# Kernel tuning notes

Measured on AMD Instinct MI355X. Metric: run time of the kernel, lower is better.

## Reference

```python
import jax, jax.numpy as jnp
import numpy as np

N_NODES = 50000
N_EDGES = 1600000
F_IN = 128
C = 64          # block in/out channels
EF = 64         # edge MLP hidden dim
BLOCKS = 3
MLP_DIM = 128
N_CLASSES = 10
N_GRAPHS = 512
EPS = 1e-5


def setup_inputs() -> dict:
    key = jax.random.key(0)
    ks = jax.random.split(key, 32)
    s = 0.05
    inp = {
        "x": jax.random.normal(ks[0], (N_NODES, F_IN), jnp.float32),
        "edge_index": jax.random.randint(ks[1], (2, N_EDGES), 0, N_NODES, jnp.int64),
        "batch": jnp.sort(jax.random.randint(ks[2], (N_NODES,), 0, N_GRAPHS, jnp.int64)),
        "fc0_w": jax.random.normal(ks[3], (F_IN, C), jnp.float32) * s,
        "fc0_b": jnp.zeros((C,), jnp.float32),
        "fc1_w": jax.random.normal(ks[4], (BLOCKS * C, MLP_DIM), jnp.float32) * s,
        "fc1_b": jnp.zeros((MLP_DIM,), jnp.float32),
        "fc2_w": jax.random.normal(ks[5], (MLP_DIM, N_CLASSES), jnp.float32) * s,
        "fc2_b": jnp.zeros((N_CLASSES,), jnp.float32),
    }
    for i in range(BLOCKS):
        k = 6 + 4 * i
        inp[f"bn_g{i}"] = jnp.ones((C,), jnp.float32)
        inp[f"bn_b{i}"] = jnp.zeros((C,), jnp.float32)
        inp[f"w1_{i}"] = jax.random.normal(ks[k], (2 * C, EF), jnp.float32) * s
        inp[f"b1_{i}"] = jnp.zeros((EF,), jnp.float32)
        inp[f"w2_{i}"] = jax.random.normal(ks[k + 1], (EF, C), jnp.float32) * s
        inp[f"b2_{i}"] = jnp.zeros((C,), jnp.float32)
    return inp


def _batchnorm(x, g, b):
    mu = jnp.mean(x, axis=0)
    var = jnp.var(x, axis=0)
    return (x - mu) * jax.lax.rsqrt(var + EPS) * g + b


def _edge_conv(x, src, dst, w1, b1, w2, b2):
    # PyG-style EdgeConv: msg = MLP(concat[x_i, x_j - x_i]), max-aggregate at i
    xi = x[dst]                                  # [E, C]
    xj = x[src]                                  # [E, C]
    h = jax.nn.relu(jnp.concatenate([xi, xj - xi], axis=-1) @ w1 + b1)  # [E, EF]
    m = h @ w2 + b2                              # [E, C]
    agg = jax.ops.segment_max(m, dst, num_segments=N_NODES)
    return jnp.where(jnp.isfinite(agg), agg, 0.0)


def reference(x, edge_index, batch, fc0_w, fc0_b, fc1_w, fc1_b, fc2_w, fc2_b,
              bn_g0, bn_b0, w1_0, b1_0, w2_0, b2_0,
              bn_g1, bn_b1, w1_1, b1_1, w2_1, b2_1,
              bn_g2, bn_b2, w1_2, b1_2, w2_2, b2_2):
    src, dst = edge_index[0], edge_index[1]
    h = x @ fc0_w + fc0_b                        # [N, C]
    blocks = [(bn_g0, bn_b0, w1_0, b1_0, w2_0, b2_0),
              (bn_g1, bn_b1, w1_1, b1_1, w2_1, b2_1),
              (bn_g2, bn_b2, w1_2, b1_2, w2_2, b2_2)]
    xs = []
    for (g, b, w1, b1, w2, b2) in blocks:
        h = _batchnorm(h, g, b)
        h = jax.nn.relu(_edge_conv(h, src, dst, w1, b1, w2, b2))
        xs.append(h)
    cat = jnp.concatenate(xs, axis=-1)           # [N, 3C]
    # global mean pool over graphs
    sums = jax.ops.segment_sum(cat, batch, num_segments=N_GRAPHS)
    cnt = jax.ops.segment_sum(jnp.ones((N_NODES,), cat.dtype), batch,
                              num_segments=N_GRAPHS)
    pooled = sums / jnp.maximum(cnt, 1.0)[:, None]   # [G, 3C]
    hid = jax.nn.relu(pooled @ fc1_w + fc1_b)
    return jax.nn.log_softmax(hid @ fc2_w + fc2_b, axis=-1)
```

## Files before the change

kernel.cpp:

```cpp
#include <hip/hip_runtime.h>
#include <math.h>

#define N_NODES 50000
#define N_TILES 3125
#define N_EDGES 1600000
#define F_IN 128
#define C 64
#define EF 64
#define N_GRAPHS 512
#define MLP_DIM 128
#define N_CLASSES 10
#define EPS 1e-5f
#define NB 196
#define CAPB 16384
#define CHUNK 4096
#define NSLICE 8

typedef __attribute__((ext_vector_type(8))) _Float16 half8;
typedef __attribute__((ext_vector_type(2))) _Float16 half2v;
typedef __attribute__((ext_vector_type(4))) float floatx4;
typedef __attribute__((ext_vector_type(4))) unsigned uintx4;

union Uh { uintx4 v; half2v h[4]; half8 h8; };

__device__ __forceinline__ unsigned short f2h(float a) {
    union { _Float16 f; unsigned short u; } c;
    c.f = (_Float16)a;
    return c.u;
}
__device__ __forceinline__ float h2f(unsigned short u) {
    union { unsigned short u; _Float16 f; } c;
    c.u = u;
    return (float)c.f;
}
__device__ __forceinline__ half2v pk2(float a, float b) {
    auto t = __builtin_amdgcn_cvt_pkrtz(a, b);
    union { decltype(t) i; half2v o; } c;
    c.i = t;
    return c.o;
}

__global__ __launch_bounds__(256) void pass1_kernel(const int* __restrict__ src,
                                                    const int* __restrict__ dst,
                                                    int* __restrict__ gcur,
                                                    unsigned* __restrict__ keys) {
    __shared__ int lcnt[NB], lbase[NB], lcnt2[NB];
    int tid = threadIdx.x;
    int e0 = blockIdx.x * CHUNK;
    unsigned k[CHUNK / 256];
    int bk[CHUNK / 256];
    for (int i = tid; i < NB; i += 256) lcnt[i] = 0;
    __syncthreads();
#pragma unroll
    for (int i = 0; i < CHUNK / 256; i++) {
        int e = e0 + i * 256 + tid;
        if (e < N_EDGES) {
            int d = dst[e];
            k[i] = ((unsigned)d << 16) | (unsigned)src[e];
            bk[i] = d >> 8;
            atomicAdd(&lcnt[bk[i]], 1);
        } else bk[i] = -1;
    }
    __syncthreads();
    for (int i = tid; i < NB; i += 256) {
        int c = lcnt[i];
        lbase[i] = c ? atomicAdd(&gcur[i], c) : 0;
        lcnt2[i] = 0;
    }
    __syncthreads();
#pragma unroll
    for (int i = 0; i < CHUNK / 256; i++) {
        if (bk[i] >= 0) {
            int r = atomicAdd(&lcnt2[bk[i]], 1);
            keys[(size_t)bk[i] * CAPB + lbase[bk[i]] + r] = k[i];
        }
    }
}

__global__ __launch_bounds__(256) void node_count_kernel(const unsigned* __restrict__ keys,
                                                         const int* __restrict__ bcnt,
                                                         int* __restrict__ cnt,
                                                         int* __restrict__ bsum) {
    __shared__ int lc[256], rs[256];
    int tid = threadIdx.x, b = blockIdx.x;
    lc[tid] = 0;
    __syncthreads();
    int beg = b * CAPB, end = beg + bcnt[b];
    for (int p = beg + tid; p < end; p += 256)
        atomicAdd(&lc[(keys[p] >> 16) & 255], 1);
    __syncthreads();
    int node = b * 256 + tid;
    int c = (node < N_NODES) ? lc[tid] : 0;
    if (node < N_NODES) cnt[node] = c;
    rs[tid] = (c + 15) & ~15;
    __syncthreads();
    for (int off = 128; off > 0; off >>= 1) {
        if (tid < off) rs[tid] += rs[tid + off];
        __syncthreads();
    }
    if (tid == 0) bsum[b] = rs[0];
}

__global__ void pscan_kernel(const int* __restrict__ bsum, int* __restrict__ bbase,
                             int* __restrict__ row_start) {
    __shared__ int a[256];
    int tid = threadIdx.x;
    int v = (tid < NB) ? bsum[tid] : 0;
    a[tid] = v;
    __syncthreads();
    for (int off = 1; off < 256; off <<= 1) {
        int t = (tid >= off) ? a[tid - off] : 0;
        __syncthreads();
        a[tid] += t;
        __syncthreads();
    }
    int excl = a[tid] - v;
    if (tid < NB) bbase[tid] = excl;
    if (tid == NB - 1) row_start[N_NODES] = excl + v;
}

__global__ __launch_bounds__(256) void pass2_kernel(const unsigned* __restrict__ keys,
                                                    const int* __restrict__ bcnt,
                                                    const int* __restrict__ cnt,
                                                    const int* __restrict__ bbase,
                                                    int* __restrict__ row_start,
                                                    unsigned short* __restrict__ sorted_src) {
    __shared__ int loc[256], rs[256], cur[256];
    int tid = threadIdx.x, b = blockIdx.x;
    int node = b * 256 + tid;
    int c = (node < N_NODES) ? cnt[node] : 0;
    int pc = (c + 15) & ~15;
    loc[tid] = pc;
    cur[tid] = 0;
    __syncthreads();
    for (int off = 1; off < 256; off <<= 1) {
        int t = (tid >= off) ? loc[tid - off] : 0;
        __syncthreads();
        loc[tid] += t;
        __syncthreads();
    }
    int myrs = bbase[b] + loc[tid] - pc;
    rs[tid] = myrs;
    if (node < N_NODES) row_start[node] = myrs;
    __syncthreads();
    int beg = b * CAPB, end = beg + bcnt[b];
    for (int p = beg + tid; p < end; p += 256) {
        unsigned k = keys[p];
        int lidx = (k >> 16) & 255;
        int r = atomicAdd(&cur[lidx], 1);
        sorted_src[rs[lidx] + r] = (unsigned short)(k & 0xFFFFu);
    }
    __syncthreads();
    if (node < N_NODES) {
        int deg = cur[tid];
        if (deg > 0) {
            unsigned short s0 = sorted_src[myrs];
            for (int p = myrs + deg; p < myrs + pc; p++) sorted_src[p] = s0;
        }
    }
}

__global__ __launch_bounds__(256, 3) void fc0_mfma_kernel(const float* __restrict__ x,
                                                          const float* __restrict__ w,
                                                          const float* __restrict__ b,
                                                          unsigned short* __restrict__ h0,
                                                          float* __restrict__ bns) {
    __shared__ float bl1[4][64], bl2[4][64];
    int tid = threadIdx.x, lane = tid & 63, wid = tid >> 6;
    int q = lane >> 4, cl = lane & 15, kq = q * 8;

    Uh wf[4][4];
#pragma unroll
    for (int kh = 0; kh < 4; kh++)
#pragma unroll
        for (int cb = 0; cb < 4; cb++)
#pragma unroll
            for (int j = 0; j < 4; j++) {
                int k0 = kh * 32 + kq + 2 * j;
                int col = cb * 16 + cl;
                wf[kh][cb].h[j] = pk2(w[k0 * 64 + col], w[(k0 + 1) * 64 + col]);
            }
    float bv[4];
#pragma unroll
    for (int cb = 0; cb < 4; cb++) bv[cb] = b[cb * 16 + cl];
    float s1[4] = {0, 0, 0, 0}, s2[4] = {0, 0, 0, 0};

    for (int t = blockIdx.x * 4 + wid; t < N_TILES; t += gridDim.x * 4) {
        int nb = t * 16;
        floatx4 acc[4] = {{0,0,0,0},{0,0,0,0},{0,0,0,0},{0,0,0,0}};
#pragma unroll
        for (int kh = 0; kh < 4; kh++) {
            const float* xr = x + (size_t)(nb + cl) * F_IN + kh * 32 + kq;
            floatx4 xa = *(const floatx4*)xr;
            floatx4 xb = *(const floatx4*)(xr + 4);
            Uh xf;
            xf.h[0] = pk2(xa.x, xa.y); xf.h[1] = pk2(xa.z, xa.w);
            xf.h[2] = pk2(xb.x, xb.y); xf.h[3] = pk2(xb.z, xb.w);
#pragma unroll
            for (int cb = 0; cb < 4; cb++)
                acc[cb] = __builtin_amdgcn_mfma_f32_16x16x32_f16(xf.h8, wf[kh][cb].h8, acc[cb], 0, 0, 0);
        }
#pragma unroll
        for (int cb = 0; cb < 4; cb++)
#pragma unroll
            for (int r = 0; r < 4; r++) {
                float v = acc[cb][r] + bv[cb];
                h0[(size_t)(nb + q * 4 + r) * 64 + cb * 16 + cl] = f2h(v);
                s1[cb] += v; s2[cb] += v * v;
            }
    }
#pragma unroll
    for (int cb = 0; cb < 4; cb++) {
        s1[cb] += __shfl_xor(s1[cb], 16); s1[cb] += __shfl_xor(s1[cb], 32);
        s2[cb] += __shfl_xor(s2[cb], 16); s2[cb] += __shfl_xor(s2[cb], 32);
    }
    if (lane < 16) {
#pragma unroll
        for (int cb = 0; cb < 4; cb++) { bl1[wid][cb * 16 + lane] = s1[cb]; bl2[wid][cb * 16 + lane] = s2[cb]; }
    }
    __syncthreads();
    if (tid < 64) {
        float a  = bl1[0][tid] + bl1[1][tid] + bl1[2][tid] + bl1[3][tid];
        float c2 = bl2[0][tid] + bl2[1][tid] + bl2[2][tid] + bl2[3][tid];
        int sl = blockIdx.x & (NSLICE - 1);
        atomicAdd(&bns[sl * 128 + tid], a);
        atomicAdd(&bns[sl * 128 + 64 + tid], c2);
    }
}

__global__ __launch_bounds__(256, 4) void ab_mfma_kernel(const unsigned short* __restrict__ h,
                                                         const float* __restrict__ bns,
                                                         const float* __restrict__ g,
                                                         const float* __restrict__ bb,
                                                         const float* __restrict__ w1,
                                                         const float* __restrict__ b1,
                                                         unsigned short* __restrict__ A,
                                                         unsigned short* __restrict__ Bb) {
    __shared__ float scale[64], shift[64], cab[128];
    int tid = threadIdx.x, lane = tid & 63, wid = tid >> 6;
    int q = lane >> 4, cl = lane & 15, kq = q * 8;

    if (tid < 64) {
        float s1v = 0.f, s2v = 0.f;
#pragma unroll
        for (int s = 0; s < NSLICE; s++) { s1v += bns[s * 128 + tid]; s2v += bns[s * 128 + 64 + tid]; }
        float mu  = s1v * (1.0f / N_NODES);
        float var = s2v * (1.0f / N_NODES) - mu * mu;
        float sc  = g[tid] * rsqrtf(var + EPS);
        scale[tid] = sc;
        shift[tid] = bb[tid] - mu * sc;
    }
    __syncthreads();
    if (tid < 128) {
        int j = tid & 63;
        float acc = (tid < 64) ? b1[j] : 0.f;
        for (int k = 0; k < 64; k++) {
            float wa_ = w1[k * EF + j], wb_ = w1[(64 + k) * EF + j];
            acc = fmaf(shift[k], (tid < 64) ? (wa_ - wb_) : wb_, acc);
        }
        cab[tid] = acc;
    }
    Uh wa[2][4], wb[2][4];
#pragma unroll
    for (int kh = 0; kh < 2; kh++)
#pragma unroll
        for (int cb = 0; cb < 4; cb++)
#pragma unroll
            for (int j = 0; j < 4; j++) {
                int k0 = kh * 32 + kq + 2 * j;
                int col = cb * 16 + cl;
                float sa = scale[k0], sb = scale[k0 + 1];
                float a0 = w1[k0 * EF + col], b0 = w1[(64 + k0) * EF + col];
                float a1 = w1[(k0 + 1) * EF + col], b1v = w1[(64 + k0 + 1) * EF + col];
                wa[kh][cb].h[j] = pk2(sa * (a0 - b0), sb * (a1 - b1v));
                wb[kh][cb].h[j] = pk2(sa * b0, sb * b1v);
            }
    __syncthreads();
    float cav[4], cbv[4];
#pragma unroll
    for (int cb = 0; cb < 4; cb++) { cav[cb] = cab[cb * 16 + cl]; cbv[cb] = cab[64 + cb * 16 + cl]; }

    for (int t = blockIdx.x * 4 + wid; t < N_TILES; t += gridDim.x * 4) {
        int nb = t * 16;
        const unsigned short* hrow = h + (size_t)(nb + cl) * 64 + kq;
        Uh h0f, h1f;
        h0f.v = *(const uintx4*)hrow;
        h1f.v = *(const uintx4*)(hrow + 32);
        floatx4 accA[4] = {{0,0,0,0},{0,0,0,0},{0,0,0,0},{0,0,0,0}};
        floatx4 accB[4] = {{0,0,0,0},{0,0,0,0},{0,0,0,0},{0,0,0,0}};
#pragma unroll
        for (int cb = 0; cb < 4; cb++) {
            accA[cb] = __builtin_amdgcn_mfma_f32_16x16x32_f16(h0f.h8, wa[0][cb].h8, accA[cb], 0, 0, 0);
            accB[cb] = __builtin_amdgcn_mfma_f32_16x16x32_f16(h0f.h8, wb[0][cb].h8, accB[cb], 0, 0, 0);
            accA[cb] = __builtin_amdgcn_mfma_f32_16x16x32_f16(h1f.h8, wa[1][cb].h8, accA[cb], 0, 0, 0);
            accB[cb] = __builtin_amdgcn_mfma_f32_16x16x32_f16(h1f.h8, wb[1][cb].h8, accB[cb], 0, 0, 0);
        }
#pragma unroll
        for (int cb = 0; cb < 4; cb++)
#pragma unroll
            for (int r = 0; r < 4; r++) {
                size_t o = (size_t)(nb + q * 4 + r) * 64 + cb * 16 + cl;
                A[o]  = f2h(accA[cb][r] + cav[cb]);
                Bb[o] = f2h(accB[cb][r] + cbv[cb]);
            }
    }
}

__global__ __launch_bounds__(256, 4) void edge_mfma_kernel(
        const unsigned short* __restrict__ A, const unsigned short* __restrict__ Bb,
        const int* __restrict__ row_start, const unsigned short* __restrict__ sorted_src,
        const float* __restrict__ w2, const float* __restrict__ b2,
        unsigned short* __restrict__ catp, float* __restrict__ bnsNext) {
    __shared__ float r1[4][64], r2[4][64];
    int tid = threadIdx.x, lane = tid & 63, wid = tid >> 6;
    int kq = (lane >> 4) * 8;
    int cl = lane & 15;

    Uh bfr[2][4];
#pragma unroll
    for (int kh = 0; kh < 2; kh++)
#pragma unroll
        for (int cb = 0; cb < 4; cb++)
#pragma unroll
            for (int j = 0; j < 4; j++) {
                _Float16 w0 = (_Float16)w2[(kh * 32 + kq + 2 * j) * 64 + cb * 16 + cl];
                _Float16 w1 = (_Float16)w2[(kh * 32 + kq + 2 * j + 1) * 64 + cb * 16 + cl];
                bfr[kh][cb].h[j] = half2v{w0, w1};
            }
    float b2j = b2[lane];
    float s1 = 0.f, s2 = 0.f;
    const half2v zeroh = {(_Float16)0.f, (_Float16)0.f};

    for (int n = blockIdx.x * 4 + wid; n < N_NODES; n += gridDim.x * 4) {
        int beg = row_start[n], end = row_start[n + 1];
        const unsigned short* arow = A + (size_t)n * 64 + kq;
        Uh a0u, a1u;
        a0u.v = *(const uintx4*)(arow);
        a1u.v = *(const uintx4*)(arow + 32);
        floatx4 rmax0 = {-INFINITY, -INFINITY, -INFINITY, -INFINITY};
        floatx4 rmax1 = rmax0, rmax2 = rmax0, rmax3 = rmax0;

        auto tile = [&](uintx4 u0, uintx4 u1) {
            Uh b0u, b1u, f0, f1;
            b0u.v = u0; b1u.v = u1;
#pragma unroll
            for (int j = 0; j < 4; j++) {
                f0.h[j] = __builtin_elementwise_max(a0u.h[j] + b0u.h[j], zeroh);
                f1.h[j] = __builtin_elementwise_max(a1u.h[j] + b1u.h[j], zeroh);
            }
            floatx4 acc0 = {0.f, 0.f, 0.f, 0.f}, acc1 = acc0, acc2 = acc0, acc3 = acc0;
            acc0 = __builtin_amdgcn_mfma_f32_16x16x32_f16(f0.h8, bfr[0][0].h8, acc0, 0, 0, 0);
            acc1 = __builtin_amdgcn_mfma_f32_16x16x32_f16(f0.h8, bfr[0][1].h8, acc1, 0, 0, 0);
            acc2 = __builtin_amdgcn_mfma_f32_16x16x32_f16(f0.h8, bfr[0][2].h8, acc2, 0, 0, 0);
            acc3 = __builtin_amdgcn_mfma_f32_16x16x32_f16(f0.h8, bfr[0][3].h8, acc3, 0, 0, 0);
            acc0 = __builtin_amdgcn_mfma_f32_16x16x32_f16(f1.h8, bfr[1][0].h8, acc0, 0, 0, 0);
            acc1 = __builtin_amdgcn_mfma_f32_16x16x32_f16(f1.h8, bfr[1][1].h8, acc1, 0, 0, 0);
            acc2 = __builtin_amdgcn_mfma_f32_16x16x32_f16(f1.h8, bfr[1][2].h8, acc2, 0, 0, 0);
            acc3 = __builtin_amdgcn_mfma_f32_16x16x32_f16(f1.h8, bfr[1][3].h8, acc3, 0, 0, 0);
            rmax0 = __builtin_elementwise_max(rmax0, acc0);
            rmax1 = __builtin_elementwise_max(rmax1, acc1);
            rmax2 = __builtin_elementwise_max(rmax2, acc2);
            rmax3 = __builtin_elementwise_max(rmax3, acc3);
        };
        auto gather = [&](int p, uintx4& u0, uintx4& u1) {
            int srcm = sorted_src[p + cl];
            const unsigned short* brow = Bb + (size_t)srcm * 64 + kq;
            u0 = *(const uintx4*)(brow);
            u1 = *(const uintx4*)(brow + 32);
        };

        int p0 = beg;
        for (; p0 + 32 <= end; p0 += 32) {
            uintx4 x0, x1, y0, y1;
            gather(p0, x0, x1);
            gather(p0 + 16, y0, y1);
            tile(x0, x1);
            tile(y0, y1);
        }
        if (p0 < end) {
            uintx4 x0, x1;
            gather(p0, x0, x1);
            tile(x0, x1);
        }

        float v0 = fmaxf(fmaxf(rmax0.x, rmax0.y), fmaxf(rmax0.z, rmax0.w));
        float v1 = fmaxf(fmaxf(rmax1.x, rmax1.y), fmaxf(rmax1.z, rmax1.w));
        float v2 = fmaxf(fmaxf(rmax2.x, rmax2.y), fmaxf(rmax2.z, rmax2.w));
        float v3 = fmaxf(fmaxf(rmax3.x, rmax3.y), fmaxf(rmax3.z, rmax3.w));
        v0 = fmaxf(v0, __shfl_xor(v0, 16)); v0 = fmaxf(v0, __shfl_xor(v0, 32));
        v1 = fmaxf(v1, __shfl_xor(v1, 16)); v1 = fmaxf(v1, __shfl_xor(v1, 32));
        v2 = fmaxf(v2, __shfl_xor(v2, 16)); v2 = fmaxf(v2, __shfl_xor(v2, 32));
        v3 = fmaxf(v3, __shfl_xor(v3, 16)); v3 = fmaxf(v3, __shfl_xor(v3, 32));
        float vs = (lane & 32) ? ((lane & 16) ? v3 : v2) : ((lane & 16) ? v1 : v0);
        float v = fmaxf(vs + b2j, 0.f);
        catp[(size_t)n * 64 + lane] = f2h(v);
        s1 += v; s2 += v * v;
    }

    if (bnsNext) {
        r1[wid][lane] = s1; r2[wid][lane] = s2;
        __syncthreads();
        if (tid < 64) {
            float a  = r1[0][tid] + r1[1][tid] + r1[2][tid] + r1[3][tid];
            float c2 = r2[0][tid] + r2[1][tid] + r2[2][tid] + r2[3][tid];
            int sl = blockIdx.x & (NSLICE - 1);
            atomicAdd(&bnsNext[sl * 128 + tid], a);
            atomicAdd(&bnsNext[sl * 128 + 64 + tid], c2);
        }
    }
}

__global__ __launch_bounds__(192) void poolhead_kernel(const unsigned short* __restrict__ cat0,
                                                       const unsigned short* __restrict__ cat1,
                                                       const unsigned short* __restrict__ cat2,
                                                       const int* __restrict__ batch,
                                                       const float* __restrict__ fc1w,
                                                       const float* __restrict__ fc1b,
                                                       const float* __restrict__ fc2w,
                                                       const float* __restrict__ fc2b,
                                                       float* __restrict__ out) {
    __shared__ int se[2];
    __shared__ float p[192];
    __shared__ float hid[128];
    __shared__ float z[10];
    __shared__ float lse;
    int g = blockIdx.x, tid = threadIdx.x;
    if (tid < 2) {
        int target = g + tid;
        int lo = 0, hi = N_NODES;
        while (lo < hi) { int mid = (lo + hi) >> 1; if (batch[mid] < target) lo = mid + 1; else hi = mid; }
        se[tid] = lo;
    }
    __syncthreads();
    int s = se[0], e = se[1];
    const unsigned short* plane = (tid < 64) ? cat0 : ((tid < 128) ? cat1 : cat2);
    int col = tid & 63;
    float acc = 0.f;
    for (int r = s; r < e; r++) acc += h2f(plane[(size_t)r * 64 + col]);
    float denom = (e > s) ? (float)(e - s) : 1.0f;
    p[tid] = acc / denom;
    __syncthreads();
    if (tid < MLP_DIM) {
        float a = fc1b[tid];
        for (int k = 0; k < 192; k++) a = fmaf(p[k], fc1w[k * 128 + tid], a);
        hid[tid] = fmaxf(a, 0.f);
    }
    __syncthreads();
    if (tid < N_CLASSES) {
        float a = fc2b[tid];
        for (int k = 0; k < 128; k++) a = fmaf(hid[k], fc2w[k * 10 + tid], a);
        z[tid] = a;
    }
    __syncthreads();
    if (tid == 0) {
        float m = z[0];
        for (int i = 1; i < 10; i++) m = fmaxf(m, z[i]);
        float sm = 0.f;
        for (int i = 0; i < 10; i++) sm += expf(z[i] - m);
        lse = m + logf(sm);
    }
    __syncthreads();
    if (tid < N_CLASSES) out[g * 10 + tid] = z[tid] - lse;
}

extern "C" void kernel_launch(void* const* d_in, const int* in_sizes, int n_in,
                              void* d_out, int out_size, void* d_ws, size_t ws_size,
                              hipStream_t stream) {
    (void)in_sizes; (void)n_in; (void)out_size; (void)ws_size;
    const float* x    = (const float*)d_in[0];
    const int*   ei   = (const int*)d_in[1];
    const int*   batch= (const int*)d_in[2];
    const float* fc0w = (const float*)d_in[3];
    const float* fc0b = (const float*)d_in[4];
    const float* fc1w = (const float*)d_in[5];
    const float* fc1b = (const float*)d_in[6];
    const float* fc2w = (const float*)d_in[7];
    const float* fc2b = (const float*)d_in[8];
    const int* src = ei;
    const int* dst = ei + N_EDGES;
    float* out = (float*)d_out;

    char* w = (char*)d_ws;
    size_t off = 0;
    auto alloc = [&](size_t bytes) -> void* {
        void* p = w + off;
        off = (off + bytes + 255) & ~(size_t)255;
        return p;
    };
    const size_t MAX_PAD_EDGES = (size_t)N_EDGES + 16 * (size_t)N_NODES;

    char* zbase = (char*)alloc(1024 + 3 * NSLICE * 128 * 4);
    int*   gcur   = (int*)zbase;
    float* bnsAll = (float*)(zbase + 1024);
    const size_t ZBYTES = 1024 + 3 * NSLICE * 128 * 4;

    unsigned short* cat0 = (unsigned short*)alloc((size_t)N_NODES * 64 * 2);
    unsigned short* cat1 = (unsigned short*)alloc((size_t)N_NODES * 64 * 2);
    unsigned short* cat2 = (unsigned short*)alloc((size_t)N_NODES * 64 * 2);
    unsigned short* h0   = (unsigned short*)alloc((size_t)N_NODES * 64 * 2);
    unsigned short* Ae   = (unsigned short*)alloc((size_t)N_NODES * 64 * 2);
    unsigned short* Be   = (unsigned short*)alloc((size_t)N_NODES * 64 * 2);
    unsigned* keys = (unsigned*)alloc((size_t)NB * CAPB * 4);
    unsigned short* sorted_src = (unsigned short*)alloc(MAX_PAD_EDGES * 2);
    int*   cnt     = (int*)alloc((size_t)N_NODES * 4);
    int*   row_start = (int*)alloc((size_t)(N_NODES + 1) * 4);
    int*   bsum    = (int*)alloc(NB * 4);
    int*   bbase   = (int*)alloc(NB * 4);

    (void)hipMemsetAsync(zbase, 0, ZBYTES, stream);

    pass1_kernel<<<(N_EDGES + CHUNK - 1) / CHUNK, 256, 0, stream>>>(src, dst, gcur, keys);
    node_count_kernel<<<NB, 256, 0, stream>>>(keys, gcur, cnt, bsum);
    pscan_kernel<<<1, 256, 0, stream>>>(bsum, bbase, row_start);
    pass2_kernel<<<NB, 256, 0, stream>>>(keys, gcur, cnt, bbase, row_start, sorted_src);

    fc0_mfma_kernel<<<782, 256, 0, stream>>>(x, fc0w, fc0b, h0, bnsAll);

    unsigned short* planes[3] = {cat0, cat1, cat2};
    for (int blk = 0; blk < 3; blk++) {
        const float* g  = (const float*)d_in[9 + 6 * blk];
        const float* bb = (const float*)d_in[10 + 6 * blk];
        const float* w1 = (const float*)d_in[11 + 6 * blk];
        const float* b1 = (const float*)d_in[12 + 6 * blk];
        const float* w2 = (const float*)d_in[13 + 6 * blk];
        const float* b2 = (const float*)d_in[14 + 6 * blk];
        const unsigned short* hsrc = (blk == 0) ? h0 : planes[blk - 1];

        ab_mfma_kernel<<<782, 256, 0, stream>>>(hsrc, bnsAll + blk * NSLICE * 128,
                                                g, bb, w1, b1, Ae, Be);
        edge_mfma_kernel<<<2048, 256, 0, stream>>>(
            Ae, Be, row_start, sorted_src, w2, b2, planes[blk],
            (blk < 2) ? (bnsAll + (blk + 1) * NSLICE * 128) : nullptr);
    }

    poolhead_kernel<<<N_GRAPHS, 192, 0, stream>>>(cat0, cat1, cat2, batch,
                                                  fc1w, fc1b, fc2w, fc2b, out);
}
```

Baseline: 428.5 us.

## Simplify CSR build with global atomics and interleave two nodes per wave in edge kernel

The CSR construction is rebuilt. Per-node degrees are counted with global atomics in pass1, and row starts come from a per-block scan whose base is claimed with an atomic. A 4-way split scatter kernel replaces the count/scan/pass2 chain, and padding slots are filled by memsetting a 0xFFFF sentinel that the gather resolves to a real neighbour. The edge kernel now has each wave process two nodes in interleaved gather/MFMA steps to expose more memory-level parallelism, and its occupancy hint is dropped. The pooling loop gets four accumulators. The cost is extra global atomic traffic, a large memset, and CSR row order that depends on atomic ordering.

```diff
diff --git a/kernel.cpp b/kernel.cpp
--- a/kernel.cpp
+++ b/kernel.cpp
@@ -43,7 +43,8 @@
 __global__ __launch_bounds__(256) void pass1_kernel(const int* __restrict__ src,
                                                     const int* __restrict__ dst,
                                                     int* __restrict__ gcur,
-                                                    unsigned* __restrict__ keys) {
+                                                    unsigned* __restrict__ keys,
+                                                    int* __restrict__ cnt) {
     __shared__ int lcnt[NB], lbase[NB], lcnt2[NB];
     int tid = threadIdx.x;
     int e0 = blockIdx.x * CHUNK;
@@ -59,6 +60,7 @@
             k[i] = ((unsigned)d << 16) | (unsigned)src[e];
             bk[i] = d >> 8;
             atomicAdd(&lcnt[bk[i]], 1);
+            atomicAdd(&cnt[d], 1);
         } else bk[i] = -1;
     }
     __syncthreads();
@@ -77,61 +79,15 @@
     }
 }
 
-__global__ __launch_bounds__(256) void node_count_kernel(const unsigned* __restrict__ keys,
-                                                         const int* __restrict__ bcnt,
-                                                         int* __restrict__ cnt,
-                                                         int* __restrict__ bsum) {
-    __shared__ int lc[256], rs[256];
-    int tid = threadIdx.x, b = blockIdx.x;
-    lc[tid] = 0;
-    __syncthreads();
-    int beg = b * CAPB, end = beg + bcnt[b];
-    for (int p = beg + tid; p < end; p += 256)
-        atomicAdd(&lc[(keys[p] >> 16) & 255], 1);
-    __syncthreads();
-    int node = b * 256 + tid;
-    int c = (node < N_NODES) ? lc[tid] : 0;
-    if (node < N_NODES) cnt[node] = c;
-    rs[tid] = (c + 15) & ~15;
-    __syncthreads();
-    for (int off = 128; off > 0; off >>= 1) {
-        if (tid < off) rs[tid] += rs[tid + off];
-        __syncthreads();
-    }
-    if (tid == 0) bsum[b] = rs[0];
-}
-
-__global__ void pscan_kernel(const int* __restrict__ bsum, int* __restrict__ bbase,
-                             int* __restrict__ row_start) {
-    __shared__ int a[256];
-    int tid = threadIdx.x;
-    int v = (tid < NB) ? bsum[tid] : 0;
-    a[tid] = v;
-    __syncthreads();
-    for (int off = 1; off < 256; off <<= 1) {
-        int t = (tid >= off) ? a[tid - off] : 0;
-        __syncthreads();
-        a[tid] += t;
-        __syncthreads();
-    }
-    int excl = a[tid] - v;
-    if (tid < NB) bbase[tid] = excl;
-    if (tid == NB - 1) row_start[N_NODES] = excl + v;
-}
-
-__global__ __launch_bounds__(256) void pass2_kernel(const unsigned* __restrict__ keys,
-                                                    const int* __restrict__ bcnt,
-                                                    const int* __restrict__ cnt,
-                                                    const int* __restrict__ bbase,
-                                                    int* __restrict__ row_start,
-                                                    unsigned short* __restrict__ sorted_src) {
-    __shared__ int loc[256], rs[256], cur[256];
+__global__ __launch_bounds__(256) void rowstart_kernel(const int* __restrict__ cnt,
+                                                       int* __restrict__ gtotal,
+                                                       int* __restrict__ row_start) {
+    __shared__ int loc[256];
+    __shared__ int base;
     int tid = threadIdx.x, b = blockIdx.x;
     int node = b * 256 + tid;
-    int c = (node < N_NODES) ? cnt[node] : 0;
-    int pc = (c + 15) & ~15;
+    int pc = (node < N_NODES) ? ((cnt[node] + 15) & ~15) : 0;
     loc[tid] = pc;
-    cur[tid] = 0;
     __syncthreads();
     for (int off = 1; off < 256; off <<= 1) {
         int t = (tid >= off) ? loc[tid - off] : 0;
@@ -139,24 +95,27 @@
         loc[tid] += t;
         __syncthreads();
     }
-    int myrs = bbase[b] + loc[tid] - pc;
-    rs[tid] = myrs;
-    if (node < N_NODES) row_start[node] = myrs;
-    __syncthreads();
-    int beg = b * CAPB, end = beg + bcnt[b];
-    for (int p = beg + tid; p < end; p += 256) {
-        unsigned k = keys[p];
-        int lidx = (k >> 16) & 255;
-        int r = atomicAdd(&cur[lidx], 1);
-        sorted_src[rs[lidx] + r] = (unsigned short)(k & 0xFFFFu);
-    }
-    __syncthreads();
-    if (node < N_NODES) {
-        int deg = cur[tid];
-        if (deg > 0) {
-            unsigned short s0 = sorted_src[myrs];
-            for (int p = myrs + deg; p < myrs + pc; p++) sorted_src[p] = s0;
-        }
+    if (tid == 255) base = atomicAdd(gtotal, loc[255]);
+    __syncthreads();
+    if (node < N_NODES) row_start[node] = base + loc[tid] - pc;
+}
+
+__global__ __launch_bounds__(256) void scatter4_kernel(const unsigned* __restrict__ keys,
+                                                       const int* __restrict__ gcur,
+                                                       const int* __restrict__ row_start,
+                                                       int* __restrict__ cursor,
+                                                       unsigned short* __restrict__ sorted_src) {
+    int b = blockIdx.x >> 2, part = blockIdx.x & 3;
+    int nk = gcur[b];
+    int chunk = (nk + 3) >> 2;
+    int beg = part * chunk;
+    int end = beg + chunk; if (end > nk) end = nk;
+    const unsigned* kb = keys + (size_t)b * CAPB;
+    for (int p = beg + threadIdx.x; p < end; p += 256) {
+        unsigned k = kb[p];
+        int d = k >> 16;
+        int r = atomicAdd(&cursor[d], 1);
+        sorted_src[row_start[d] + r] = (unsigned short)(k & 0xFFFFu);
     }
 }
 
@@ -306,12 +265,13 @@
     }
 }
 
-__global__ __launch_bounds__(256, 4) void edge_mfma_kernel(
+__global__ __launch_bounds__(256) void edge_mfma_kernel(
         const unsigned short* __restrict__ A, const unsigned short* __restrict__ Bb,
-        const int* __restrict__ row_start, const unsigned short* __restrict__ sorted_src,
+        const int* __restrict__ row_start, const int* __restrict__ cnt,
+        const unsigned short* __restrict__ sorted_src,
         const float* __restrict__ w2, const float* __restrict__ b2,
         unsigned short* __restrict__ catp, float* __restrict__ bnsNext) {
-    __shared__ float r1[4][64], r2[4][64];
+    __shared__ float r1s[4][64], r2s[4][64];
     int tid = threadIdx.x, lane = tid & 63, wid = tid >> 6;
     int kq = (lane >> 4) * 8;
     int cl = lane & 15;
@@ -331,78 +291,83 @@
     float s1 = 0.f, s2 = 0.f;
     const half2v zeroh = {(_Float16)0.f, (_Float16)0.f};
 
-    for (int n = blockIdx.x * 4 + wid; n < N_NODES; n += gridDim.x * 4) {
-        int beg = row_start[n], end = row_start[n + 1];
-        const unsigned short* arow = A + (size_t)n * 64 + kq;
-        Uh a0u, a1u;
-        a0u.v = *(const uintx4*)(arow);
-        a1u.v = *(const uintx4*)(arow + 32);
-        floatx4 rmax0 = {-INFINITY, -INFINITY, -INFINITY, -INFINITY};
-        floatx4 rmax1 = rmax0, rmax2 = rmax0, rmax3 = rmax0;
-
-        auto tile = [&](uintx4 u0, uintx4 u1) {
+    auto gather = [&](int p, uintx4& u0, uintx4& u1) {
+        int srcm = sorted_src[p + cl];
+        int ent0 = __shfl(srcm, lane & 48);
+        srcm = (srcm == 0xFFFF) ? ent0 : srcm;
+        const unsigned short* brow = Bb + (size_t)srcm * 64 + kq;
+        u0 = *(const uintx4*)(brow);
+        u1 = *(const uintx4*)(brow + 32);
+    };
+
+    for (int nb = blockIdx.x * 8 + wid * 2; nb < N_NODES; nb += gridDim.x * 8) {
+        int n0 = nb, n1 = nb + 1;
+        int rs0 = row_start[n0], rs1 = row_start[n1];
+        int e0p = rs0 + ((cnt[n0] + 15) & ~15);
+        int e1p = rs1 + ((cnt[n1] + 15) & ~15);
+        const unsigned short* ar0 = A + (size_t)n0 * 64 + kq;
+        const unsigned short* ar1 = A + (size_t)n1 * 64 + kq;
+        Uh a00, a01, a10, a11;
+        a00.v = *(const uintx4*)ar0; a01.v = *(const uintx4*)(ar0 + 32);
+        a10.v = *(const uintx4*)ar1; a11.v = *(const uintx4*)(ar1 + 32);
+        floatx4 rm0[4], rm1[4];
+#pragma unroll
+        for (int i = 0; i < 4; i++) {
+            rm0[i] = floatx4{-INFINITY, -INFINITY, -INFINITY, -INFINITY};
+            rm1[i] = rm0[i];
+        }
+
+        auto tile = [&](Uh& aa0, Uh& aa1, floatx4 (&rm)[4], uintx4 u0, uintx4 u1) {
             Uh b0u, b1u, f0, f1;
             b0u.v = u0; b1u.v = u1;
 #pragma unroll
             for (int j = 0; j < 4; j++) {
-                f0.h[j] = __builtin_elementwise_max(a0u.h[j] + b0u.h[j], zeroh);
-                f1.h[j] = __builtin_elementwise_max(a1u.h[j] + b1u.h[j], zeroh);
-            }
-            floatx4 acc0 = {0.f, 0.f, 0.f, 0.f}, acc1 = acc0, acc2 = acc0, acc3 = acc0;
-            acc0 = __builtin_amdgcn_mfma_f32_16x16x32_f16(f0.h8, bfr[0][0].h8, acc0, 0, 0, 0);
-            acc1 = __builtin_amdgcn_mfma_f32_16x16x32_f16(f0.h8, bfr[0][1].h8, acc1, 0, 0, 0);
-            acc2 = __builtin_amdgcn_mfma_f32_16x16x32_f16(f0.h8, bfr[0][2].h8, acc2, 0, 0, 0);
-            acc3 = __builtin_amdgcn_mfma_f32_16x16x32_f16(f0.h8, bfr[0][3].h8, acc3, 0, 0, 0);
-            acc0 = __builtin_amdgcn_mfma_f32_16x16x32_f16(f1.h8, bfr[1][0].h8, acc0, 0, 0, 0);
-            acc1 = __builtin_amdgcn_mfma_f32_16x16x32_f16(f1.h8, bfr[1][1].h8, acc1, 0, 0, 0);
-            acc2 = __builtin_amdgcn_mfma_f32_16x16x32_f16(f1.h8, bfr[1][2].h8, acc2, 0, 0, 0);
-            acc3 = __builtin_amdgcn_mfma_f32_16x16x32_f16(f1.h8, bfr[1][3].h8, acc3, 0, 0, 0);
-            rmax0 = __builtin_elementwise_max(rmax0, acc0);
-            rmax1 = __builtin_elementwise_max(rmax1, acc1);
-            rmax2 = __builtin_elementwise_max(rmax2, acc2);
-            rmax3 = __builtin_elementwise_max(rmax3, acc3);
+                f0.h[j] = __builtin_elementwise_max(aa0.h[j] + b0u.h[j], zeroh);
+                f1.h[j] = __builtin_elementwise_max(aa1.h[j] + b1u.h[j], zeroh);
+            }
+#pragma unroll
+            for (int cb = 0; cb < 4; cb++) {
+                floatx4 acc = {0.f, 0.f, 0.f, 0.f};
+                acc = __builtin_amdgcn_mfma_f32_16x16x32_f16(f0.h8, bfr[0][cb].h8, acc, 0, 0, 0);
+                acc = __builtin_amdgcn_mfma_f32_16x16x32_f16(f1.h8, bfr[1][cb].h8, acc, 0, 0, 0);
+                rm[cb] = __builtin_elementwise_max(rm[cb], acc);
+            }
         };
-        auto gather = [&](int p, uintx4& u0, uintx4& u1) {
-            int srcm = sorted_src[p + cl];
-            const unsigned short* brow = Bb + (size_t)srcm * 64 + kq;
-            u0 = *(const uintx4*)(brow);
-            u1 = *(const uintx4*)(brow + 32);
+
+        int p0 = rs0, p1 = rs1;
+        while (p0 < e0p || p1 < e1p) {
+            uintx4 x0, x1, y0, y1;
+            bool d0 = p0 < e0p, d1 = p1 < e1p;
+            if (d0) gather(p0, x0, x1);
+            if (d1) gather(p1, y0, y1);
+            if (d0) { tile(a00, a01, rm0, x0, x1); p0 += 16; }
+            if (d1) { tile(a10, a11, rm1, y0, y1); p1 += 16; }
+        }
+
+        auto finish = [&](floatx4 (&rm)[4], int n) {
+            float v0 = fmaxf(fmaxf(rm[0].x, rm[0].y), fmaxf(rm[0].z, rm[0].w));
+            float v1 = fmaxf(fmaxf(rm[1].x, rm[1].y), fmaxf(rm[1].z, rm[1].w));
+            float v2 = fmaxf(fmaxf(rm[2].x, rm[2].y), fmaxf(rm[2].z, rm[2].w));
+            float v3 = fmaxf(fmaxf(rm[3].x, rm[3].y), fmaxf(rm[3].z, rm[3].w));
+            v0 = fmaxf(v0, __shfl_xor(v0, 16)); v0 = fmaxf(v0, __shfl_xor(v0, 32));
+            v1 = fmaxf(v1, __shfl_xor(v1, 16)); v1 = fmaxf(v1, __shfl_xor(v1, 32));
+            v2 = fmaxf(v2, __shfl_xor(v2, 16)); v2 = fmaxf(v2, __shfl_xor(v2, 32));
+            v3 = fmaxf(v3, __shfl_xor(v3, 16)); v3 = fmaxf(v3, __shfl_xor(v3, 32));
+            float vs = (lane & 32) ? ((lane & 16) ? v3 : v2) : ((lane & 16) ? v1 : v0);
+            float v = fmaxf(vs + b2j, 0.f);
+            catp[(size_t)n * 64 + lane] = f2h(v);
+            s1 += v; s2 += v * v;
         };
-
-        int p0 = beg;
-        for (; p0 + 32 <= end; p0 += 32) {
-            uintx4 x0, x1, y0, y1;
-            gather(p0, x0, x1);
-            gather(p0 + 16, y0, y1);
-            tile(x0, x1);
-            tile(y0, y1);
-        }
-        if (p0 < end) {
-            uintx4 x0, x1;
-            gather(p0, x0, x1);
-            tile(x0, x1);
-        }
-
-        float v0 = fmaxf(fmaxf(rmax0.x, rmax0.y), fmaxf(rmax0.z, rmax0.w));
-        float v1 = fmaxf(fmaxf(rmax1.x, rmax1.y), fmaxf(rmax1.z, rmax1.w));
-        float v2 = fmaxf(fmaxf(rmax2.x, rmax2.y), fmaxf(rmax2.z, rmax2.w));
-        float v3 = fmaxf(fmaxf(rmax3.x, rmax3.y), fmaxf(rmax3.z, rmax3.w));
-        v0 = fmaxf(v0, __shfl_xor(v0, 16)); v0 = fmaxf(v0, __shfl_xor(v0, 32));
-        v1 = fmaxf(v1, __shfl_xor(v1, 16)); v1 = fmaxf(v1, __shfl_xor(v1, 32));
-        v2 = fmaxf(v2, __shfl_xor(v2, 16)); v2 = fmaxf(v2, __shfl_xor(v2, 32));
-        v3 = fmaxf(v3, __shfl_xor(v3, 16)); v3 = fmaxf(v3, __shfl_xor(v3, 32));
-        float vs = (lane & 32) ? ((lane & 16) ? v3 : v2) : ((lane & 16) ? v1 : v0);
-        float v = fmaxf(vs + b2j, 0.f);
-        catp[(size_t)n * 64 + lane] = f2h(v);
-        s1 += v; s2 += v * v;
+        finish(rm0, n0);
+        finish(rm1, n1);
     }
 
     if (bnsNext) {
-        r1[wid][lane] = s1; r2[wid][lane] = s2;
+        r1s[wid][lane] = s1; r2s[wid][lane] = s2;
         __syncthreads();
         if (tid < 64) {
-            float a  = r1[0][tid] + r1[1][tid] + r1[2][tid] + r1[3][tid];
-            float c2 = r2[0][tid] + r2[1][tid] + r2[2][tid] + r2[3][tid];
+            float a  = r1s[0][tid] + r1s[1][tid] + r1s[2][tid] + r1s[3][tid];
+            float c2 = r2s[0][tid] + r2s[1][tid] + r2s[2][tid] + r2s[3][tid];
             int sl = blockIdx.x & (NSLICE - 1);
             atomicAdd(&bnsNext[sl * 128 + tid], a);
             atomicAdd(&bnsNext[sl * 128 + 64 + tid], c2);
@@ -435,8 +400,16 @@
     int s = se[0], e = se[1];
     const unsigned short* plane = (tid < 64) ? cat0 : ((tid < 128) ? cat1 : cat2);
     int col = tid & 63;
-    float acc = 0.f;
-    for (int r = s; r < e; r++) acc += h2f(plane[(size_t)r * 64 + col]);
+    float a0 = 0.f, a1 = 0.f, a2 = 0.f, a3 = 0.f;
+    int r = s;
+    for (; r + 4 <= e; r += 4) {
+        a0 += h2f(plane[(size_t)(r + 0) * 64 + col]);
+        a1 += h2f(plane[(size_t)(r + 1) * 64 + col]);
+        a2 += h2f(plane[(size_t)(r + 2) * 64 + col]);
+        a3 += h2f(plane[(size_t)(r + 3) * 64 + col]);
+    }
+    for (; r < e; r++) a0 += h2f(plane[(size_t)r * 64 + col]);
+    float acc = (a0 + a1) + (a2 + a3);
     float denom = (e > s) ? (float)(e - s) : 1.0f;
     p[tid] = acc / denom;
     __syncthreads();
@@ -489,10 +462,16 @@
     };
     const size_t MAX_PAD_EDGES = (size_t)N_EDGES + 16 * (size_t)N_NODES;
 
-    char* zbase = (char*)alloc(1024 + 3 * NSLICE * 128 * 4);
+    const size_t BNS_OFF = 1280;
+    const size_t CNT_OFF = BNS_OFF + 3 * NSLICE * 128 * 4;
+    const size_t CUR_OFF = CNT_OFF + (size_t)N_NODES * 4;
+    const size_t ZBYTES  = CUR_OFF + (size_t)N_NODES * 4;
+    char* zbase = (char*)alloc(ZBYTES);
     int*   gcur   = (int*)zbase;
-    float* bnsAll = (float*)(zbase + 1024);
-    const size_t ZBYTES = 1024 + 3 * NSLICE * 128 * 4;
+    int*   gtotal = (int*)(zbase + 1024);
+    float* bnsAll = (float*)(zbase + BNS_OFF);
+    int*   cnt    = (int*)(zbase + CNT_OFF);
+    int*   cursor = (int*)(zbase + CUR_OFF);
 
     unsigned short* cat0 = (unsigned short*)alloc((size_t)N_NODES * 64 * 2);
     unsigned short* cat1 = (unsigned short*)alloc((size_t)N_NODES * 64 * 2);
@@ -502,17 +481,14 @@
     unsigned short* Be   = (unsigned short*)alloc((size_t)N_NODES * 64 * 2);
     unsigned* keys = (unsigned*)alloc((size_t)NB * CAPB * 4);
     unsigned short* sorted_src = (unsigned short*)alloc(MAX_PAD_EDGES * 2);
-    int*   cnt     = (int*)alloc((size_t)N_NODES * 4);
-    int*   row_start = (int*)alloc((size_t)(N_NODES + 1) * 4);
-    int*   bsum    = (int*)alloc(NB * 4);
-    int*   bbase   = (int*)alloc(NB * 4);
+    int*   row_start = (int*)alloc((size_t)N_NODES * 4);
 
     (void)hipMemsetAsync(zbase, 0, ZBYTES, stream);
-
-    pass1_kernel<<<(N_EDGES + CHUNK - 1) / CHUNK, 256, 0, stream>>>(src, dst, gcur, keys);
-    node_count_kernel<<<NB, 256, 0, stream>>>(keys, gcur, cnt, bsum);
-    pscan_kernel<<<1, 256, 0, stream>>>(bsum, bbase, row_start);
-    pass2_kernel<<<NB, 256, 0, stream>>>(keys, gcur, cnt, bbase, row_start, sorted_src);
+    (void)hipMemsetAsync(sorted_src, 0xFF, MAX_PAD_EDGES * 2, stream);
+
+    pass1_kernel<<<(N_EDGES + CHUNK - 1) / CHUNK, 256, 0, stream>>>(src, dst, gcur, keys, cnt);
+    rowstart_kernel<<<NB, 256, 0, stream>>>(cnt, gtotal, row_start);
+    scatter4_kernel<<<NB * 4, 256, 0, stream>>>(keys, gcur, row_start, cursor, sorted_src);
 
     fc0_mfma_kernel<<<782, 256, 0, stream>>>(x, fc0w, fc0b, h0, bnsAll);
 
@@ -529,7 +505,7 @@
         ab_mfma_kernel<<<782, 256, 0, stream>>>(hsrc, bnsAll + blk * NSLICE * 128,
                                                 g, bb, w1, b1, Ae, Be);
         edge_mfma_kernel<<<2048, 256, 0, stream>>>(
-            Ae, Be, row_start, sorted_src, w2, b2, planes[blk],
+            Ae, Be, row_start, cnt, sorted_src, w2, b2, planes[blk],
             (blk < 2) ? (bnsAll + (blk + 1) * NSLICE * 128) : nullptr);
     }
 
```

Measured after the change: 545.7 us. 1.27x slower.

## Process two destination nodes per wave in edge kernel, unroll pooling sums

Applied to the files above, without the earlier changes.

Each wave in the edge MFMA kernel now handles two adjacent destination nodes at once, interleaving their neighbor gathers and MFMA tiles so more independent memory loads are in flight. This aims to hide gather latency that a single node with few 16-edge tiles could not cover. The launch-bounds occupancy hint is dropped, which may let register use grow and lower occupancy. The pooling kernel's per-column sum is split into four independent accumulators to shorten the dependent add chain.

```diff
diff --git a/kernel.cpp b/kernel.cpp
--- a/kernel.cpp
+++ b/kernel.cpp
@@ -306,12 +306,12 @@
     }
 }
 
-__global__ __launch_bounds__(256, 4) void edge_mfma_kernel(
+__global__ __launch_bounds__(256) void edge_mfma_kernel(
         const unsigned short* __restrict__ A, const unsigned short* __restrict__ Bb,
         const int* __restrict__ row_start, const unsigned short* __restrict__ sorted_src,
         const float* __restrict__ w2, const float* __restrict__ b2,
         unsigned short* __restrict__ catp, float* __restrict__ bnsNext) {
-    __shared__ float r1[4][64], r2[4][64];
+    __shared__ float r1s[4][64], r2s[4][64];
     int tid = threadIdx.x, lane = tid & 63, wid = tid >> 6;
     int kq = (lane >> 4) * 8;
     int cl = lane & 15;
@@ -331,78 +331,80 @@
     float s1 = 0.f, s2 = 0.f;
     const half2v zeroh = {(_Float16)0.f, (_Float16)0.f};
 
-    for (int n = blockIdx.x * 4 + wid; n < N_NODES; n += gridDim.x * 4) {
-        int beg = row_start[n], end = row_start[n + 1];
-        const unsigned short* arow = A + (size_t)n * 64 + kq;
-        Uh a0u, a1u;
-        a0u.v = *(const uintx4*)(arow);
-        a1u.v = *(const uintx4*)(arow + 32);
-        floatx4 rmax0 = {-INFINITY, -INFINITY, -INFINITY, -INFINITY};
-        floatx4 rmax1 = rmax0, rmax2 = rmax0, rmax3 = rmax0;
-
-        auto tile = [&](uintx4 u0, uintx4 u1) {
+    auto gather = [&](int p, uintx4& u0, uintx4& u1) {
+        int srcm = sorted_src[p + cl];
+        const unsigned short* brow = Bb + (size_t)srcm * 64 + kq;
+        u0 = *(const uintx4*)(brow);
+        u1 = *(const uintx4*)(brow + 32);
+    };
+
+    for (int nb = blockIdx.x * 8 + wid * 2; nb < N_NODES; nb += gridDim.x * 8) {
+        int n0 = nb, n1 = nb + 1;
+        int rs0 = row_start[n0], e0p = row_start[n0 + 1];
+        int rs1 = e0p,           e1p = row_start[n1 + 1];
+        const unsigned short* ar0 = A + (size_t)n0 * 64 + kq;
+        const unsigned short* ar1 = A + (size_t)n1 * 64 + kq;
+        Uh a00, a01, a10, a11;
+        a00.v = *(const uintx4*)ar0; a01.v = *(const uintx4*)(ar0 + 32);
+        a10.v = *(const uintx4*)ar1; a11.v = *(const uintx4*)(ar1 + 32);
+        floatx4 rm0[4], rm1[4];
+#pragma unroll
+        for (int i = 0; i < 4; i++) {
+            rm0[i] = floatx4{-INFINITY, -INFINITY, -INFINITY, -INFINITY};
+            rm1[i] = rm0[i];
+        }
+
+        auto tile = [&](Uh& aa0, Uh& aa1, floatx4 (&rm)[4], uintx4 u0, uintx4 u1) {
             Uh b0u, b1u, f0, f1;
             b0u.v = u0; b1u.v = u1;
 #pragma unroll
             for (int j = 0; j < 4; j++) {
-                f0.h[j] = __builtin_elementwise_max(a0u.h[j] + b0u.h[j], zeroh);
-                f1.h[j] = __builtin_elementwise_max(a1u.h[j] + b1u.h[j], zeroh);
-            }
-            floatx4 acc0 = {0.f, 0.f, 0.f, 0.f}, acc1 = acc0, acc2 = acc0, acc3 = acc0;
-            acc0 = __builtin_amdgcn_mfma_f32_16x16x32_f16(f0.h8, bfr[0][0].h8, acc0, 0, 0, 0);
-            acc1 = __builtin_amdgcn_mfma_f32_16x16x32_f16(f0.h8, bfr[0][1].h8, acc1, 0, 0, 0);
-            acc2 = __builtin_amdgcn_mfma_f32_16x16x32_f16(f0.h8, bfr[0][2].h8, acc2, 0, 0, 0);
-            acc3 = __builtin_amdgcn_mfma_f32_16x16x32_f16(f0.h8, bfr[0][3].h8, acc3, 0, 0, 0);
-            acc0 = __builtin_amdgcn_mfma_f32_16x16x32_f16(f1.h8, bfr[1][0].h8, acc0, 0, 0, 0);
-            acc1 = __builtin_amdgcn_mfma_f32_16x16x32_f16(f1.h8, bfr[1][1].h8, acc1, 0, 0, 0);
-            acc2 = __builtin_amdgcn_mfma_f32_16x16x32_f16(f1.h8, bfr[1][2].h8, acc2, 0, 0, 0);
-            acc3 = __builtin_amdgcn_mfma_f32_16x16x32_f16(f1.h8, bfr[1][3].h8, acc3, 0, 0, 0);
-            rmax0 = __builtin_elementwise_max(rmax0, acc0);
-            rmax1 = __builtin_elementwise_max(rmax1, acc1);
-            rmax2 = __builtin_elementwise_max(rmax2, acc2);
-            rmax3 = __builtin_elementwise_max(rmax3, acc3);
+                f0.h[j] = __builtin_elementwise_max(aa0.h[j] + b0u.h[j], zeroh);
+                f1.h[j] = __builtin_elementwise_max(aa1.h[j] + b1u.h[j], zeroh);
+            }
+#pragma unroll
+            for (int cb = 0; cb < 4; cb++) {
+                floatx4 acc = {0.f, 0.f, 0.f, 0.f};
+                acc = __builtin_amdgcn_mfma_f32_16x16x32_f16(f0.h8, bfr[0][cb].h8, acc, 0, 0, 0);
+                acc = __builtin_amdgcn_mfma_f32_16x16x32_f16(f1.h8, bfr[1][cb].h8, acc, 0, 0, 0);
+                rm[cb] = __builtin_elementwise_max(rm[cb], acc);
+            }
         };
-        auto gather = [&](int p, uintx4& u0, uintx4& u1) {
-            int srcm = sorted_src[p + cl];
-            const unsigned short* brow = Bb + (size_t)srcm * 64 + kq;
-            u0 = *(const uintx4*)(brow);
-            u1 = *(const uintx4*)(brow + 32);
+
+        int p0 = rs0, p1 = rs1;
+        while (p0 < e0p || p1 < e1p) {
+            uintx4 x0, x1, y0, y1;
+            bool d0 = p0 < e0p, d1 = p1 < e1p;
+            if (d0) gather(p0, x0, x1);
+            if (d1) gather(p1, y0, y1);
+            if (d0) { tile(a00, a01, rm0, x0, x1); p0 += 16; }
+            if (d1) { tile(a10, a11, rm1, y0, y1); p1 += 16; }
+        }
+
+        auto finish = [&](floatx4 (&rm)[4], int n) {
+            float v0 = fmaxf(fmaxf(rm[0].x, rm[0].y), fmaxf(rm[0].z, rm[0].w));
+            float v1 = fmaxf(fmaxf(rm[1].x, rm[1].y), fmaxf(rm[1].z, rm[1].w));
+            float v2 = fmaxf(fmaxf(rm[2].x, rm[2].y), fmaxf(rm[2].z, rm[2].w));
+            float v3 = fmaxf(fmaxf(rm[3].x, rm[3].y), fmaxf(rm[3].z, rm[3].w));
+            v0 = fmaxf(v0, __shfl_xor(v0, 16)); v0 = fmaxf(v0, __shfl_xor(v0, 32));
+            v1 = fmaxf(v1, __shfl_xor(v1, 16)); v1 = fmaxf(v1, __shfl_xor(v1, 32));
+            v2 = fmaxf(v2, __shfl_xor(v2, 16)); v2 = fmaxf(v2, __shfl_xor(v2, 32));
+            v3 = fmaxf(v3, __shfl_xor(v3, 16)); v3 = fmaxf(v3, __shfl_xor(v3, 32));
+            float vs = (lane & 32) ? ((lane & 16) ? v3 : v2) : ((lane & 16) ? v1 : v0);
+            float v = fmaxf(vs + b2j, 0.f);
+            catp[(size_t)n * 64 + lane] = f2h(v);
+            s1 += v; s2 += v * v;
         };
-
-        int p0 = beg;
-        for (; p0 + 32 <= end; p0 += 32) {
-            uintx4 x0, x1, y0, y1;
-            gather(p0, x0, x1);
-            gather(p0 + 16, y0, y1);
-            tile(x0, x1);
-            tile(y0, y1);
-        }
-        if (p0 < end) {
-            uintx4 x0, x1;
-            gather(p0, x0, x1);
-            tile(x0, x1);
-        }
-
-        float v0 = fmaxf(fmaxf(rmax0.x, rmax0.y), fmaxf(rmax0.z, rmax0.w));
-        float v1 = fmaxf(fmaxf(rmax1.x, rmax1.y), fmaxf(rmax1.z, rmax1.w));
-        float v2 = fmaxf(fmaxf(rmax2.x, rmax2.y), fmaxf(rmax2.z, rmax2.w));
-        float v3 = fmaxf(fmaxf(rmax3.x, rmax3.y), fmaxf(rmax3.z, rmax3.w));
-        v0 = fmaxf(v0, __shfl_xor(v0, 16)); v0 = fmaxf(v0, __shfl_xor(v0, 32));
-        v1 = fmaxf(v1, __shfl_xor(v1, 16)); v1 = fmaxf(v1, __shfl_xor(v1, 32));
-        v2 = fmaxf(v2, __shfl_xor(v2, 16)); v2 = fmaxf(v2, __shfl_xor(v2, 32));
-        v3 = fmaxf(v3, __shfl_xor(v3, 16)); v3 = fmaxf(v3, __shfl_xor(v3, 32));
-        float vs = (lane & 32) ? ((lane & 16) ? v3 : v2) : ((lane & 16) ? v1 : v0);
-        float v = fmaxf(vs + b2j, 0.f);
-        catp[(size_t)n * 64 + lane] = f2h(v);
-        s1 += v; s2 += v * v;
+        finish(rm0, n0);
+        finish(rm1, n1);
     }
 
     if (bnsNext) {
-        r1[wid][lane] = s1; r2[wid][lane] = s2;
+        r1s[wid][lane] = s1; r2s[wid][lane] = s2;
         __syncthreads();
         if (tid < 64) {
-            float a  = r1[0][tid] + r1[1][tid] + r1[2][tid] + r1[3][tid];
-            float c2 = r2[0][tid] + r2[1][tid] + r2[2][tid] + r2[3][tid];
+            float a  = r1s[0][tid] + r1s[1][tid] + r1s[2][tid] + r1s[3][tid];
+            float c2 = r2s[0][tid] + r2s[1][tid] + r2s[2][tid] + r2s[3][tid];
             int sl = blockIdx.x & (NSLICE - 1);
             atomicAdd(&bnsNext[sl * 128 + tid], a);
             atomicAdd(&bnsNext[sl * 128 + 64 + tid], c2);
@@ -435,8 +437,16 @@
     int s = se[0], e = se[1];
     const unsigned short* plane = (tid < 64) ? cat0 : ((tid < 128) ? cat1 : cat2);
     int col = tid & 63;
-    float acc = 0.f;
-    for (int r = s; r < e; r++) acc += h2f(plane[(size_t)r * 64 + col]);
+    float a0 = 0.f, a1 = 0.f, a2 = 0.f, a3 = 0.f;
+    int r = s;
+    for (; r + 4 <= e; r += 4) {
+        a0 += h2f(plane[(size_t)(r + 0) * 64 + col]);
+        a1 += h2f(plane[(size_t)(r + 1) * 64 + col]);
+        a2 += h2f(plane[(size_t)(r + 2) * 64 + col]);
+        a3 += h2f(plane[(size_t)(r + 3) * 64 + col]);
+    }
+    for (; r < e; r++) a0 += h2f(plane[(size_t)r * 64 + col]);
+    float acc = (a0 + a1) + (a2 + a3);
     float denom = (e > s) ? (float)(e - s) : 1.0f;
     p[tid] = acc / denom;
     __syncthreads();
```

New measurement: 468.5 us. 1.09x slower.
